# Kernel tuning notes

Measured on AMD Instinct MI355X. Metric: run time of the kernel, lower is better.

Reference implementation:

```python
import jax, jax.numpy as jnp
import numpy as np

EPS = 1e-5  # torch LayerNorm default


def _layer_norm(x, g, b):
    mu = jnp.mean(x, axis=-1, keepdims=True)
    var = jnp.mean(jnp.square(x - mu), axis=-1, keepdims=True)
    return (x - mu) * jax.lax.rsqrt(var + EPS) * g + b


def setup_inputs() -> dict:
    key = jax.random.key(0)
    ks = jax.random.split(key, 8)
    B, S, D = 4, 2048, 1024
    s = 1.0 / np.sqrt(D)
    return {
        "q": jax.random.normal(ks[0], (B, S, D), jnp.float32),
        "k": jax.random.normal(ks[1], (B, S, D), jnp.float32),
        "v": jax.random.normal(ks[2], (B, S, D), jnp.float32),
        "mask": jnp.ones((B, 1, S), jnp.int32),
        "Wq": jax.random.normal(ks[3], (D, D), jnp.float32) * s,
        "Wk": jax.random.normal(ks[4], (D, D), jnp.float32) * s,
        "Wv": jax.random.normal(ks[5], (D, D), jnp.float32) * s,
        "Wo": jax.random.normal(ks[6], (D, D), jnp.float32) * s,
        "ln_q_g": jnp.ones((D,), jnp.float32),
        "ln_q_b": jnp.zeros((D,), jnp.float32),
        "ln_k_g": jnp.ones((D,), jnp.float32),
        "ln_k_b": jnp.zeros((D,), jnp.float32),
        "ln_v_g": jnp.ones((D,), jnp.float32),
        "ln_v_b": jnp.zeros((D,), jnp.float32),
    }


def reference(q, k, v, mask, Wq, Wk, Wv, Wo,
              ln_q_g, ln_q_b, ln_k_g, ln_k_b, ln_v_g, ln_v_b):
    B, Lq, D = q.shape
    H = 16
    dk = D // H
    residual = q
    # pre-LN + bias-free projections
    qh = (_layer_norm(q, ln_q_g, ln_q_b) @ Wq).reshape(B, Lq, H, dk).transpose(0, 2, 1, 3)
    kh = (_layer_norm(k, ln_k_g, ln_k_b) @ Wk).reshape(B, -1, H, dk).transpose(0, 2, 1, 3)
    vh = (_layer_norm(v, ln_v_g, ln_v_b) @ Wv).reshape(B, -1, H, dk).transpose(0, 2, 1, 3)
    # scaled scores [B,H,Lq,Lk]
    scores = jnp.einsum('bhqd,bhkd->bhqk', qh, kh) / jnp.sqrt(jnp.float32(dk))
    pad = (mask == 0)[:, None, :, :]  # [B,1,*,Lk], True where masked
    scores = jnp.where(pad, -jnp.inf, scores)
    attn = jax.nn.softmax(scores, axis=-1)
    attn = jnp.where(pad, 0.0, attn)
    out = jnp.einsum('bhqk,bhkd->bhqd', attn, vh)
    out = out.transpose(0, 2, 1, 3).reshape(B, Lq, D)
    return out @ Wo + residual
```

## Files before the change

kernel.cpp:

```cpp
#include <hip/hip_runtime.h>
#include <stdint.h>

typedef __attribute__((ext_vector_type(8))) short short8;
typedef __attribute__((ext_vector_type(4))) float f32x4;
typedef __attribute__((ext_vector_type(4))) unsigned short us4;

#define B_ 4
#define S_ 2048
#define D_ 1024
#define H_ 16
#define DK_ 64

__device__ __forceinline__ unsigned short f2bf(float f) {
  union { float f; unsigned int u; } c; c.f = f;
  unsigned int r = (c.u + 0x7fffu + ((c.u >> 16) & 1u)) >> 16;
  return (unsigned short)r;
}

__device__ __forceinline__ unsigned int cvt_pk_bf16(float lo, float hi) {
  unsigned int r;
  asm("v_cvt_pk_bf16_f32 %0, %1, %2" : "=v"(r) : "v"(lo), "v"(hi));
  return r;
}

__device__ __forceinline__ float exp2_fast(float x) {
#if __has_builtin(__builtin_amdgcn_exp2f)
  return __builtin_amdgcn_exp2f(x);
#else
  float r; asm("v_exp_f32 %0, %1" : "=v"(r) : "v"(x)); return r;
#endif
}

__device__ __forceinline__ void glds16(const void* g, void* l) {
  __builtin_amdgcn_global_load_lds(
      (__attribute__((address_space(1))) void*)(uintptr_t)g,
      (__attribute__((address_space(3))) void*)l, 16, 0, 0);
}

__device__ __forceinline__ f32x4 mfma_bf16(short8 a, short8 b, f32x4 c) {
  return __builtin_amdgcn_mfma_f32_16x16x32_bf16(a, b, c, 0, 0, 0);
}

__global__ __launch_bounds__(256) void ln_bf16_3(const float* __restrict__ x0,
                                                 const float* __restrict__ x1,
                                                 const float* __restrict__ x2,
                                                 const float* __restrict__ g0,
                                                 const float* __restrict__ g1,
                                                 const float* __restrict__ g2,
                                                 const float* __restrict__ b0,
                                                 const float* __restrict__ b1,
                                                 const float* __restrict__ b2,
                                                 unsigned short* __restrict__ y0,
                                                 unsigned short* __restrict__ y1,
                                                 unsigned short* __restrict__ y2) {
  const int which = blockIdx.y;
  const float* x = which == 0 ? x0 : (which == 1 ? x1 : x2);
  const float* g = which == 0 ? g0 : (which == 1 ? g1 : g2);
  const float* bta = which == 0 ? b0 : (which == 1 ? b1 : b2);
  unsigned short* y = which == 0 ? y0 : (which == 1 ? y1 : y2);

  const int lane = threadIdx.x & 63, wid = threadIdx.x >> 6;
  const int row = blockIdx.x * 4 + wid;
  const float4* xr = (const float4*)(x + (size_t)row * D_);
  float4 v[4];
  float s1 = 0.f, s2 = 0.f;
#pragma unroll
  for (int i = 0; i < 4; ++i) {
    v[i] = xr[i * 64 + lane];
    s1 += v[i].x + v[i].y + v[i].z + v[i].w;
    s2 += v[i].x * v[i].x + v[i].y * v[i].y + v[i].z * v[i].z + v[i].w * v[i].w;
  }
#pragma unroll
  for (int m = 32; m; m >>= 1) { s1 += __shfl_xor(s1, m); s2 += __shfl_xor(s2, m); }
  const float mu = s1 * (1.f / D_);
  const float inv = rsqrtf(s2 * (1.f / D_) - mu * mu + 1e-5f);
  const float4* gp = (const float4*)g;
  const float4* bp = (const float4*)bta;
  us4* yr = (us4*)(y + (size_t)row * D_);
#pragma unroll
  for (int i = 0; i < 4; ++i) {
    float4 gv = gp[i * 64 + lane], bv = bp[i * 64 + lane];
    us4 o;
    o[0] = f2bf((v[i].x - mu) * inv * gv.x + bv.x);
    o[1] = f2bf((v[i].y - mu) * inv * gv.y + bv.y);
    o[2] = f2bf((v[i].z - mu) * inv * gv.z + bv.z);
    o[3] = f2bf((v[i].w - mu) * inv * gv.w + bv.w);
    yr[i * 64 + lane] = o;
  }
}

__global__ void wt_bf16_4(const float* __restrict__ W0, const float* __restrict__ W1,
                          const float* __restrict__ W2, const float* __restrict__ W3,
                          unsigned short* __restrict__ T0, unsigned short* __restrict__ T1,
                          unsigned short* __restrict__ T2, unsigned short* __restrict__ T3) {
  const int which = blockIdx.z;
  const float* W = which == 0 ? W0 : (which == 1 ? W1 : (which == 2 ? W2 : W3));
  unsigned short* Wt = which == 0 ? T0 : (which == 1 ? T1 : (which == 2 ? T2 : T3));
  __shared__ float t[32][33];
  const int n0 = blockIdx.x * 32, k0 = blockIdx.y * 32;
  const int tx = threadIdx.x, ty = threadIdx.y;
  for (int i = ty; i < 32; i += 8) t[i][tx] = W[(size_t)(k0 + i) * D_ + n0 + tx];
  __syncthreads();
  for (int i = ty; i < 32; i += 8)
    Wt[(size_t)(n0 + i) * D_ + k0 + tx] = f2bf(t[tx][i]);
}

__global__ __launch_bounds__(256, 2) void gemm_qkv(const unsigned short* __restrict__ Xq,
                                                   const unsigned short* __restrict__ Xk,
                                                   const unsigned short* __restrict__ Xv,
                                                   const unsigned short* __restrict__ Wq,
                                                   const unsigned short* __restrict__ Wk,
                                                   const unsigned short* __restrict__ Wv,
                                                   unsigned short* __restrict__ Qh,
                                                   unsigned short* __restrict__ Kh,
                                                   unsigned short* __restrict__ Vtb,
                                                   float qscale) {
  constexpr int K = D_;
  constexpr int NT = K / 64;
  __shared__ __attribute__((aligned(16))) unsigned short As[2][128][64];
  __shared__ __attribute__((aligned(16))) unsigned short Bs[2][128][64];
  const int z = blockIdx.z;
  const unsigned short* A = z == 0 ? Xq : (z == 1 ? Xk : Xv);
  const unsigned short* Bt = z == 0 ? Wq : (z == 1 ? Wk : Wv);
  const int tid = threadIdx.x;
  const int lane = tid & 63, wid = tid >> 6;
  const int lo16 = lane & 15, hi4 = lane >> 4;
  const int wr = wid >> 1, wc = wid & 1;
  const int gx = (int)gridDim.x;
  const int lid = (int)blockIdx.x + gx * (int)blockIdx.y;
  const int nwg = gx * (int)gridDim.y;
  const int swid = (lid & 7) * (nwg >> 3) + (lid >> 3);
  const int mbase = (swid / gx) * 128, nbase = (swid % gx) * 128;
  const int srow = lane >> 3, scol = (lane & 7) * 8;

  f32x4 acc[4][4] = {};

  auto stage = [&](int bufi, int kt) {
    const int kb = kt * 64;
#pragma unroll
    for (int c = 0; c < 4; ++c) {
      const int ch = wid * 4 + c;
      glds16(A + (size_t)(mbase + ch * 8 + srow) * K + kb + scol,
             (unsigned short*)&As[bufi][0][0] + ch * 512);
      glds16(Bt + (size_t)(nbase + ch * 8 + srow) * K + kb + scol,
             (unsigned short*)&Bs[bufi][0][0] + ch * 512);
    }
  };

  stage(0, 0);
  int cur = 0;

  for (int kt = 0; kt < NT; ++kt) {
    __syncthreads();
    if (kt + 1 < NT) stage(cur ^ 1, kt + 1);
    const unsigned short* Ap = &As[cur][0][0];
    const unsigned short* Bp = &Bs[cur][0][0];
    __builtin_amdgcn_s_setprio(1);
#pragma unroll
    for (int kk = 0; kk < 2; ++kk) {
      short8 af[4], bfr[4];
#pragma unroll
      for (int i = 0; i < 4; ++i)
        af[i] = *(const short8*)(Ap + (wr * 64 + i * 16 + lo16) * 64 + kk * 32 + hi4 * 8);
#pragma unroll
      for (int j = 0; j < 4; ++j)
        bfr[j] = *(const short8*)(Bp + (wc * 64 + j * 16 + lo16) * 64 + kk * 32 + hi4 * 8);
#pragma unroll
      for (int i = 0; i < 4; ++i)
#pragma unroll
        for (int j = 0; j < 4; ++j) acc[i][j] = mfma_bf16(af[i], bfr[j], acc[i][j]);
    }
    __builtin_amdgcn_s_setprio(0);
    cur ^= 1;
  }

  if (z < 2) {
    unsigned short* out = z == 0 ? Qh : Kh;
    const float scale = z == 0 ? qscale : 1.0f;
#pragma unroll
    for (int i = 0; i < 4; ++i) {
      const int row = mbase + wr * 64 + i * 16 + hi4 * 4;
      const int b = row >> 11, s = row & (S_ - 1);
#pragma unroll
      for (int j = 0; j < 4; ++j) {
        const int col = nbase + wc * 64 + j * 16 + lo16;
        const int h = col >> 6, d = col & 63;
        const size_t base = ((size_t)(b * H_ + h) * S_ + s) * DK_ + d;
#pragma unroll
        for (int r = 0; r < 4; ++r) out[base + (size_t)r * DK_] = f2bf(acc[i][j][r] * scale);
      }
    }
  } else {
#pragma unroll
    for (int i = 0; i < 4; ++i) {
      const int row = mbase + wr * 64 + i * 16 + hi4 * 4;
      const int b = row >> 11, s0 = row & (S_ - 1);
#pragma unroll
      for (int j = 0; j < 4; ++j) {
        const int col = nbase + wc * 64 + j * 16 + lo16;
        const int h = col >> 6, d = col & 63;
        us4 w;
#pragma unroll
        for (int r = 0; r < 4; ++r) w[r] = f2bf(acc[i][j][r]);
        *(us4*)(Vtb + ((size_t)(b * H_ + h) * DK_ + d) * S_ + s0) = w;
      }
    }
  }
}

__global__ __launch_bounds__(256, 2) void gemm_out(const unsigned short* __restrict__ A,
                                                   const unsigned short* __restrict__ Bt,
                                                   float* __restrict__ out,
                                                   const float* __restrict__ resid) {
  constexpr int K = D_;
  constexpr int NT = K / 64;
  __shared__ __attribute__((aligned(16))) unsigned short As[2][128][64];
  __shared__ __attribute__((aligned(16))) unsigned short Bs[2][128][64];
  const int tid = threadIdx.x;
  const int lane = tid & 63, wid = tid >> 6;
  const int lo16 = lane & 15, hi4 = lane >> 4;
  const int wr = wid >> 1, wc = wid & 1;
  const int gx = (int)gridDim.x;
  const int lid = (int)blockIdx.x + gx * (int)blockIdx.y;
  const int nwg = gx * (int)gridDim.y;
  const int swid = (lid & 7) * (nwg >> 3) + (lid >> 3);
  const int mbase = (swid / gx) * 128, nbase = (swid % gx) * 128;
  const int srow = lane >> 3, scol = (lane & 7) * 8;

  f32x4 acc[4][4] = {};

  auto stage = [&](int bufi, int kt) {
    const int kb = kt * 64;
#pragma unroll
    for (int c = 0; c < 4; ++c) {
      const int ch = wid * 4 + c;
      glds16(A + (size_t)(mbase + ch * 8 + srow) * K + kb + scol,
             (unsigned short*)&As[bufi][0][0] + ch * 512);
      glds16(Bt + (size_t)(nbase + ch * 8 + srow) * K + kb + scol,
             (unsigned short*)&Bs[bufi][0][0] + ch * 512);
    }
  };

  stage(0, 0);
  int cur = 0;

  for (int kt = 0; kt < NT; ++kt) {
    __syncthreads();
    if (kt + 1 < NT) stage(cur ^ 1, kt + 1);
    const unsigned short* Ap = &As[cur][0][0];
    const unsigned short* Bp = &Bs[cur][0][0];
    __builtin_amdgcn_s_setprio(1);
#pragma unroll
    for (int kk = 0; kk < 2; ++kk) {
      short8 af[4], bfr[4];
#pragma unroll
      for (int i = 0; i < 4; ++i)
        af[i] = *(const short8*)(Ap + (wr * 64 + i * 16 + lo16) * 64 + kk * 32 + hi4 * 8);
#pragma unroll
      for (int j = 0; j < 4; ++j)
        bfr[j] = *(const short8*)(Bp + (wc * 64 + j * 16 + lo16) * 64 + kk * 32 + hi4 * 8);
#pragma unroll
      for (int i = 0; i < 4; ++i)
#pragma unroll
        for (int j = 0; j < 4; ++j) acc[i][j] = mfma_bf16(af[i], bfr[j], acc[i][j]);
    }
    __builtin_amdgcn_s_setprio(0);
    cur ^= 1;
  }

#pragma unroll
  for (int i = 0; i < 4; ++i) {
    const int row = mbase + wr * 64 + i * 16 + hi4 * 4;
#pragma unroll
    for (int j = 0; j < 4; ++j) {
      const int col = nbase + wc * 64 + j * 16 + lo16;
      const size_t idx = (size_t)row * D_ + col;
#pragma unroll
      for (int r = 0; r < 4; ++r)
        out[idx + (size_t)r * D_] = acc[i][j][r] + resid[idx + (size_t)r * D_];
    }
  }
}

__global__ __launch_bounds__(512, 2) void attn_k(const unsigned short* __restrict__ Qh,
                                                 const unsigned short* __restrict__ Kh,
                                                 const unsigned short* __restrict__ Vt,
                                                 const int* __restrict__ mask,
                                                 unsigned short* __restrict__ O) {
  __shared__ __attribute__((aligned(16))) unsigned short Ks[2][64][64];
  __shared__ __attribute__((aligned(16))) unsigned short Vs[2][64][64];
  __shared__ __attribute__((aligned(16))) unsigned short Ps[256][64];
  __shared__ unsigned short MskL[S_];
  __shared__ unsigned char TileOk[S_ / 64];
  const int tid = threadIdx.x, lane = tid & 63, wid = tid >> 6;
  const int lo16 = lane & 15, hi4 = lane >> 4;
  const int swz = (lo16 & 7) << 3;
  const int lid = (int)blockIdx.x + 8 * (int)blockIdx.y;
  const int swid = (lid & 7) * 64 + (lid >> 3);
  const int qb = swid & 7, bh = swid >> 3;
  const int b = bh >> 4, h = bh & 15;
  const unsigned short* Qb = Qh + (size_t)bh * S_ * DK_;
  const unsigned short* Kb = Kh + (size_t)bh * S_ * DK_;
  const unsigned short* Vb = Vt + (size_t)bh * DK_ * S_;
  const int* mb = mask + b * S_;
  const int srow = lane >> 3;
  const int scolx = ((lane & 7) ^ srow) * 8;

  for (int t = tid; t < S_; t += 512) MskL[t] = (unsigned short)(mb[t] != 0);
  __syncthreads();
  if (tid < S_ / 64) {
    int ok = 1;
    for (int j = 0; j < 64; ++j) ok &= (int)MskL[tid * 64 + j];
    TileOk[tid] = (unsigned char)ok;
  }

  short8 qf[2][2];
#pragma unroll
  for (int i = 0; i < 2; ++i)
#pragma unroll
    for (int kk = 0; kk < 2; ++kk)
      qf[i][kk] = *(const short8*)(Qb + (size_t)(qb * 256 + wid * 32 + i * 16 + lo16) * DK_ +
                                   kk * 32 + hi4 * 8);

  f32x4 o[2][4] = {};
  float lsum0 = 0.f, lsum1 = 0.f;

  auto stageKV = [&](int bufi, int kt) {
    glds16(Kb + (size_t)(kt * 64 + wid * 8 + srow) * DK_ + scolx,
           (unsigned short*)&Ks[bufi][0][0] + wid * 512);
    glds16(Vb + (size_t)(wid * 8 + srow) * S_ + kt * 64 + scolx,
           (unsigned short*)&Vs[bufi][0][0] + wid * 512);
  };

  stageKV(0, 0);
  int cur = 0;

  for (int kt = 0; kt < S_ / 64; ++kt) {
    __syncthreads();
    if (kt + 1 < S_ / 64) stageKV(cur ^ 1, kt + 1);

    const unsigned short* Kc = &Ks[cur][0][0];
    const int tok = (int)TileOk[kt];
#pragma unroll
    for (int i = 0; i < 2; ++i) {
      f32x4 p[4] = {};
      __builtin_amdgcn_s_setprio(1);
#pragma unroll
      for (int kk = 0; kk < 2; ++kk)
#pragma unroll
        for (int nf = 0; nf < 4; ++nf) {
          short8 kf = *(const short8*)(Kc + (nf * 16 + lo16) * 64 + ((kk * 32 + hi4 * 8) ^ swz));
          p[nf] = mfma_bf16(kf, qf[i][kk], p[nf]);
        }
      __builtin_amdgcn_s_setprio(0);
      if (!tok) {
#pragma unroll
        for (int nf = 0; nf < 4; ++nf) {
          const us4 mk = *(const us4*)&MskL[kt * 64 + nf * 16 + hi4 * 4];
#pragma unroll
          for (int r = 0; r < 4; ++r)
            if (!mk[r]) p[nf][r] = -1e30f;
        }
      }
      const int prow = wid * 32 + i * 16 + lo16;
      float ls = 0.f;
#pragma unroll
      for (int nf = 0; nf < 4; ++nf) {
        float e0 = exp2_fast(p[nf][0]);
        float e1 = exp2_fast(p[nf][1]);
        float e2 = exp2_fast(p[nf][2]);
        float e3 = exp2_fast(p[nf][3]);
        ls += (e0 + e1) + (e2 + e3);
        uint2 w;
        w.x = cvt_pk_bf16(e0, e1);
        w.y = cvt_pk_bf16(e2, e3);
        *(uint2*)&Ps[prow][(nf * 16 + hi4 * 4) ^ swz] = w;
      }
      if (i == 0) lsum0 += ls; else lsum1 += ls;
    }
    asm volatile("s_waitcnt lgkmcnt(0)" ::: "memory");
    __builtin_amdgcn_sched_barrier(0);
    const unsigned short* Vc = &Vs[cur][0][0];
    __builtin_amdgcn_s_setprio(1);
#pragma unroll
    for (int kk = 0; kk < 2; ++kk) {
      const int pc = (kk * 32 + hi4 * 8) ^ swz;
      short8 pa0 = *(const short8*)((const unsigned short*)Ps + (wid * 32 + 0 + lo16) * 64 + pc);
      short8 pa1 = *(const short8*)((const unsigned short*)Ps + (wid * 32 + 16 + lo16) * 64 + pc);
#pragma unroll
      for (int df = 0; df < 4; ++df) {
        short8 vf = *(const short8*)(Vc + (df * 16 + lo16) * 64 + pc);
        o[0][df] = mfma_bf16(pa0, vf, o[0][df]);
        o[1][df] = mfma_bf16(pa1, vf, o[1][df]);
      }
    }
    __builtin_amdgcn_s_setprio(0);
    cur ^= 1;
  }

  lsum0 += __shfl_xor(lsum0, 16); lsum0 += __shfl_xor(lsum0, 32);
  lsum1 += __shfl_xor(lsum1, 16); lsum1 += __shfl_xor(lsum1, 32);
#pragma unroll
  for (int i = 0; i < 2; ++i) {
#pragma unroll
    for (int r = 0; r < 4; ++r) {
      const int ql = hi4 * 4 + r;
      const float l = __shfl(i == 0 ? lsum0 : lsum1, ql);
      const float rl = l > 0.f ? 1.f / l : 0.f;
      const int srowg = qb * 256 + wid * 32 + i * 16 + ql;
      const size_t base = ((size_t)b * S_ + srowg) * D_ + h * 64;
#pragma unroll
      for (int df = 0; df < 4; ++df) O[base + df * 16 + lo16] = f2bf(o[i][df][r] * rl);
    }
  }
}

extern "C" void kernel_launch(void* const* d_in, const int* in_sizes, int n_in,
                              void* d_out, int out_size, void* d_ws, size_t ws_size,
                              hipStream_t stream) {
  const float* q = (const float*)d_in[0];
  const float* k = (const float*)d_in[1];
  const float* v = (const float*)d_in[2];
  const int* mask = (const int*)d_in[3];
  const float* Wq = (const float*)d_in[4];
  const float* Wk = (const float*)d_in[5];
  const float* Wv = (const float*)d_in[6];
  const float* Wo = (const float*)d_in[7];
  const float* lnqg = (const float*)d_in[8];
  const float* lnqb = (const float*)d_in[9];
  const float* lnkg = (const float*)d_in[10];
  const float* lnkb = (const float*)d_in[11];
  const float* lnvg = (const float*)d_in[12];
  const float* lnvb = (const float*)d_in[13];

  uint8_t* ws = (uint8_t*)d_ws;
  const size_t MB = 1024ull * 1024ull;
  unsigned short* Xq = (unsigned short*)(ws + 0 * MB);
  unsigned short* Xk = (unsigned short*)(ws + 16 * MB);
  unsigned short* Xv = (unsigned short*)(ws + 32 * MB);
  unsigned short* Wqt = (unsigned short*)(ws + 48 * MB);
  unsigned short* Wkt = (unsigned short*)(ws + 50 * MB);
  unsigned short* Wvt = (unsigned short*)(ws + 52 * MB);
  unsigned short* Wot = (unsigned short*)(ws + 54 * MB);
  unsigned short* Qh = (unsigned short*)(ws + 56 * MB);
  unsigned short* Kh = (unsigned short*)(ws + 72 * MB);
  unsigned short* Vtb = Xq;
  unsigned short* Ob = Xk;

  hipLaunchKernelGGL(wt_bf16_4, dim3(32, 32, 4), dim3(32, 8), 0, stream,
                     Wq, Wk, Wv, Wo, Wqt, Wkt, Wvt, Wot);

  hipLaunchKernelGGL(ln_bf16_3, dim3(2048, 3), dim3(256), 0, stream,
                     q, k, v, lnqg, lnkg, lnvg, lnqb, lnkb, lnvb, Xq, Xk, Xv);

  const float qscale = 0.125f * 1.4426950408889634f;
  hipLaunchKernelGGL(gemm_qkv, dim3(D_ / 128, (B_ * S_) / 128, 3), dim3(256), 0, stream,
                     Xq, Xk, Xv, Wqt, Wkt, Wvt, Qh, Kh, Vtb, qscale);

  hipLaunchKernelGGL(attn_k, dim3(S_ / 256, B_ * H_), dim3(512), 0, stream, Qh, Kh, Vtb, mask, Ob);

  hipLaunchKernelGGL(gemm_out, dim3(D_ / 128, (B_ * S_) / 128), dim3(256), 0, stream,
                     Ob, Wot, (float*)d_out, q);
}
```

Baseline: 219.3 us.

## Shrink attention LDS by reusing a per-wave P buffer and dropping mask staging

The attention kernel now does the PV product right after each 16-row score block. This lets each wave reuse one 16-row slice of the P buffer, halving its shared-memory footprint. The per-element mask copy in LDS is removed: tile validity is computed directly from global memory, and partial tiles read the mask from global during masking. The goal is lower LDS use, which could allow more resident blocks. The cost is that V fragments are reloaded for each row block and masked tiles take slower global reads.

```diff
diff --git a/kernel.cpp b/kernel.cpp
--- a/kernel.cpp
+++ b/kernel.cpp
@@ -289,9 +289,8 @@
                                                  unsigned short* __restrict__ O) {
   __shared__ __attribute__((aligned(16))) unsigned short Ks[2][64][64];
   __shared__ __attribute__((aligned(16))) unsigned short Vs[2][64][64];
-  __shared__ __attribute__((aligned(16))) unsigned short Ps[256][64];
-  __shared__ unsigned short MskL[S_];
-  __shared__ unsigned char TileOk[S_ / 64];
+  __shared__ __attribute__((aligned(16))) unsigned short Ps[128][64];
+  __shared__ int TileOkI[S_ / 64];
   const int tid = threadIdx.x, lane = tid & 63, wid = tid >> 6;
   const int lo16 = lane & 15, hi4 = lane >> 4;
   const int swz = (lo16 & 7) << 3;
@@ -306,12 +305,13 @@
   const int srow = lane >> 3;
   const int scolx = ((lane & 7) ^ srow) * 8;
 
-  for (int t = tid; t < S_; t += 512) MskL[t] = (unsigned short)(mb[t] != 0);
+  if (tid < S_ / 64) TileOkI[tid] = 1;
   __syncthreads();
-  if (tid < S_ / 64) {
-    int ok = 1;
-    for (int j = 0; j < 64; ++j) ok &= (int)MskL[tid * 64 + j];
-    TileOk[tid] = (unsigned char)ok;
+  {
+    int okp = 1;
+#pragma unroll
+    for (int j = 0; j < 4; ++j) okp &= (mb[tid * 4 + j] != 0);
+    if (!okp) TileOkI[tid >> 4] = 0;
   }
 
   short8 qf[2][2];
@@ -340,7 +340,8 @@
     if (kt + 1 < S_ / 64) stageKV(cur ^ 1, kt + 1);
 
     const unsigned short* Kc = &Ks[cur][0][0];
-    const int tok = (int)TileOk[kt];
+    const unsigned short* Vc = &Vs[cur][0][0];
+    const int tok = TileOkI[kt];
 #pragma unroll
     for (int i = 0; i < 2; ++i) {
       f32x4 p[4] = {};
@@ -355,14 +356,12 @@
       __builtin_amdgcn_s_setprio(0);
       if (!tok) {
 #pragma unroll
-        for (int nf = 0; nf < 4; ++nf) {
-          const us4 mk = *(const us4*)&MskL[kt * 64 + nf * 16 + hi4 * 4];
+        for (int nf = 0; nf < 4; ++nf)
 #pragma unroll
           for (int r = 0; r < 4; ++r)
-            if (!mk[r]) p[nf][r] = -1e30f;
-        }
+            if (mb[kt * 64 + nf * 16 + hi4 * 4 + r] == 0) p[nf][r] = -1e30f;
       }
-      const int prow = wid * 32 + i * 16 + lo16;
+      const int prow = wid * 16 + lo16;
       float ls = 0.f;
 #pragma unroll
       for (int nf = 0; nf < 4; ++nf) {
@@ -377,24 +376,21 @@
         *(uint2*)&Ps[prow][(nf * 16 + hi4 * 4) ^ swz] = w;
       }
       if (i == 0) lsum0 += ls; else lsum1 += ls;
-    }
-    asm volatile("s_waitcnt lgkmcnt(0)" ::: "memory");
-    __builtin_amdgcn_sched_barrier(0);
-    const unsigned short* Vc = &Vs[cur][0][0];
-    __builtin_amdgcn_s_setprio(1);
-#pragma unroll
-    for (int kk = 0; kk < 2; ++kk) {
-      const int pc = (kk * 32 + hi4 * 8) ^ swz;
-      short8 pa0 = *(const short8*)((const unsigned short*)Ps + (wid * 32 + 0 + lo16) * 64 + pc);
-      short8 pa1 = *(const short8*)((const unsigned short*)Ps + (wid * 32 + 16 + lo16) * 64 + pc);
-#pragma unroll
-      for (int df = 0; df < 4; ++df) {
-        short8 vf = *(const short8*)(Vc + (df * 16 + lo16) * 64 + pc);
-        o[0][df] = mfma_bf16(pa0, vf, o[0][df]);
-        o[1][df] = mfma_bf16(pa1, vf, o[1][df]);
+      asm volatile("s_waitcnt lgkmcnt(0)" ::: "memory");
+      __builtin_amdgcn_sched_barrier(0);
+      __builtin_amdgcn_s_setprio(1);
+#pragma unroll
+      for (int kk = 0; kk < 2; ++kk) {
+        const int pc = (kk * 32 + hi4 * 8) ^ swz;
+        short8 pa = *(const short8*)((const unsigned short*)Ps + (wid * 16 + lo16) * 64 + pc);
+#pragma unroll
+        for (int df = 0; df < 4; ++df) {
+          short8 vf = *(const short8*)(Vc + (df * 16 + lo16) * 64 + pc);
+          o[i][df] = mfma_bf16(pa, vf, o[i][df]);
+        }
       }
-    }
-    __builtin_amdgcn_s_setprio(0);
+      __builtin_amdgcn_s_setprio(0);
+    }
     cur ^= 1;
   }
 
```

Result: no change. 219.1 us (-0.1%).
